# Optimization experiments

Measured on AMD Instinct MI355X. Metric: run time of the kernel, lower is better.

The kernel has to match this reference:

```python
import jax, jax.numpy as jnp
import numpy as np

B, L, D, H, OUT = 4, 2048, 1024, 8, 256
DH = D // H
EPS = 1e-12


def setup_inputs() -> dict:
    key = jax.random.key(0)
    ks = jax.random.split(key, 20)
    s = lambda fan_in: 1.0 / np.sqrt(fan_in)
    def lin(k, fin, fout):
        k1, k2 = jax.random.split(k)
        w = jax.random.uniform(k1, (fin, fout), jnp.float32, -s(fin), s(fin))
        b = jax.random.uniform(k2, (fout,), jnp.float32, -s(fin), s(fin))
        return w, b
    x = jax.random.normal(ks[0], (B, L, D), jnp.float32)
    wq, bq = lin(ks[1], D, D)
    wk, bk = lin(ks[2], D, D)
    wv, bv = lin(ks[3], D, D)
    gamma = jnp.ones((D,), jnp.float32)
    beta = jnp.zeros((D,), jnp.float32)
    wff, bff = lin(ks[4], D, D)
    wc1, bc1 = lin(ks[5], D, D)
    wc2, bc2 = lin(ks[6], D, 1)
    wl1, bl1 = lin(ks[7], L, L)
    wl2, bl2 = lin(ks[8], L, OUT)
    return dict(x=x, wq=wq, bq=bq, wk=wk, bk=bk, wv=wv, bv=bv,
                gamma=gamma, beta=beta, wff=wff, bff=bff,
                wc1=wc1, bc1=bc1, wc2=wc2, bc2=bc2,
                wl1=wl1, bl1=bl1, wl2=wl2, bl2=bl2)


def layernorm(x, gamma, beta):
    mean = x.mean(-1, keepdims=True)
    var = ((x - mean) ** 2).mean(-1, keepdims=True)  # biased variance
    return gamma * (x - mean) / jnp.sqrt(var + EPS) + beta


def reference(x, wq, bq, wk, bk, wv, bv, gamma, beta, wff, bff,
              wc1, bc1, wc2, bc2, wl1, bl1, wl2, bl2):
    # multi-head self-attention (dropout = identity at inference)
    q = (x @ wq + bq).reshape(B, L, H, DH)
    k = (x @ wk + bk).reshape(B, L, H, DH)
    v = (x @ wv + bv).reshape(B, L, H, DH)
    scores = jnp.einsum('bqhd,bkhd->bhqk', q, k) / np.sqrt(DH)
    attn = jax.nn.softmax(scores, axis=-1)                  # [B,H,L,L]
    ctx = jnp.einsum('bhqk,bkhd->bqhd', attn, v).reshape(B, L, D)
    h = layernorm(x + ctx, gamma, beta)
    # feedforward: Linear + ReLU (hidden = d_model), residual + same layernorm params
    ff = jax.nn.relu(h @ wff + bff)
    h = layernorm(h + ff, gamma, beta)
    # collapse d_model -> 1
    c = jax.nn.relu(h @ wc1 + bc1)
    c = jax.nn.relu(c @ wc2 + bc2)                          # [B,L,1]
    c = jnp.squeeze(c, axis=-1)                             # [B,L]
    # collapse length -> out_featuresize
    c = jax.nn.relu(c @ wl1 + bl1)
    out = c @ wl2 + bl2                                     # [B,OUT]
    return out
```

## Files before the change

### kernel.cpp

```cpp
#include <hip/hip_runtime.h>

typedef unsigned short u16;
typedef unsigned int u32;
typedef __attribute__((ext_vector_type(4))) float f32x4;
typedef __attribute__((ext_vector_type(8))) short short8;
typedef __attribute__((ext_vector_type(4))) u32 u32x4;
typedef __attribute__((ext_vector_type(4))) u16 u16x4;

#define BB 4
#define LL 2048
#define DD 1024
#define HH 8
#define DHH 128

__device__ __forceinline__ u16 f2b(float f) {
  u32 u = __builtin_bit_cast(u32, f);
  u += 0x7fffu + ((u >> 16) & 1u);
  return (u16)(u >> 16);
}
__device__ __forceinline__ float b2f(u16 h) {
  u32 u = ((u32)h) << 16;
  return __builtin_bit_cast(float, u);
}
__device__ __forceinline__ float exp2_fast(float x) {
  float r;
  asm("v_exp_f32 %0, %1" : "=v"(r) : "v"(x));
  return r;
}
__device__ __forceinline__ u32 packbf(float a, float b) {
  return (u32)f2b(a) | ((u32)f2b(b) << 16);
}
__device__ __forceinline__ u32 bperm(int srcLane, u32 v) {
  return (u32)__builtin_amdgcn_ds_bpermute(srcLane << 2, (int)v);
}

#define GLDS16(g, l)                                                          \
  __builtin_amdgcn_global_load_lds(                                           \
      (const __attribute__((address_space(1))) void*)(g),                     \
      (__attribute__((address_space(3))) void*)(l), 16, 0, 0)

__global__ __launch_bounds__(256) void cvt_k(const float* __restrict__ X,
                                             u16* __restrict__ Xb, long n) {
  long i = ((long)blockIdx.x * 256 + threadIdx.x) * 4;
  if (i >= n) return;
  f32x4 v = *(const f32x4*)(X + i);
  u16x4 o;
#pragma unroll
  for (int k = 0; k < 4; k++) o[k] = f2b(v[k]);
  *(u16x4*)(Xb + i) = o;
}

__global__ __launch_bounds__(256) void tr_k(const float* __restrict__ W,
                                            u16* __restrict__ WT) {
  __shared__ float tile[32][33];
  const int bx = blockIdx.x, by = blockIdx.y;
  const int tx = threadIdx.x & 31, ty = threadIdx.x >> 5;
#pragma unroll
  for (int i = 0; i < 4; i++)
    tile[ty + i * 8][tx] =
        W[(long)(by * 32 + ty + i * 8) * 1024 + bx * 32 + tx];
  __syncthreads();
#pragma unroll
  for (int i = 0; i < 4; i++)
    WT[(long)(bx * 32 + ty + i * 8) * 1024 + by * 32 + tx] =
        f2b(tile[tx][ty + i * 8]);
}

__global__ __launch_bounds__(256, 3) void qkv_k(
    const u16* __restrict__ A, const u16* __restrict__ QT,
    const u16* __restrict__ KT, const u16* __restrict__ VTw,
    const float* __restrict__ bq, const float* __restrict__ bk,
    const float* __restrict__ bv, float qscale, u16* __restrict__ Qo,
    u16* __restrict__ Ko, u16* __restrict__ Vo) {
  __shared__ u16 As[2][128 * 32];
  __shared__ u16 Bs[2][128 * 32];
  const int K = 1024;
  const int nwg = gridDim.x * gridDim.y;
  const int bid = blockIdx.x + blockIdx.y * gridDim.x;
  const int swz = (bid & 7) * (nwg >> 3) + (bid >> 3);
  const int bxi = swz % 24, byi = swz / 24;
  const int sector = bxi >> 3;
  const u16* BT = sector == 0 ? QT : (sector == 1 ? KT : VTw);
  const float* bias = sector == 0 ? bq : (sector == 1 ? bk : bv);
  const float scale = sector == 0 ? qscale : 1.f;
  const int t = threadIdx.x;
  const int l = t & 63, w = t >> 6;
  const int lr = l & 15, lg = l >> 4;
  const int wr = (w >> 1) * 64, wc = (w & 1) * 64;
  const long bm = (long)byi * 128, bn = (long)(bxi & 7) * 128;
  const int srow = l >> 2;
  const int scol = (l & 3) * 8;
  const u16* Ag0 = A + (bm + w * 32 + srow) * (long)K + scol;
  const u16* Ag1 = A + (bm + w * 32 + 16 + srow) * (long)K + scol;
  const u16* Bg0 = BT + (bn + w * 32 + srow) * (long)K + scol;
  const u16* Bg1 = BT + (bn + w * 32 + 16 + srow) * (long)K + scol;
  const int wo = w * 1024;
  f32x4 acc[4][4] = {};
  GLDS16(Ag0, &As[0][wo]);
  GLDS16(Ag1, &As[0][wo + 512]);
  GLDS16(Bg0, &Bs[0][wo]);
  GLDS16(Bg1, &Bs[0][wo + 512]);
  __syncthreads();
  int cur = 0;
  for (int k0 = 0; k0 < K; k0 += 32) {
    const int nxt = cur ^ 1;
    if (k0 + 32 < K) {
      GLDS16(Ag0 + k0 + 32, &As[nxt][wo]);
      GLDS16(Ag1 + k0 + 32, &As[nxt][wo + 512]);
      GLDS16(Bg0 + k0 + 32, &Bs[nxt][wo]);
      GLDS16(Bg1 + k0 + 32, &Bs[nxt][wo + 512]);
    }
    short8 af[4], bf[4];
#pragma unroll
    for (int i = 0; i < 4; i++)
      af[i] = *(const short8*)&As[cur][(wr + i * 16 + lr) * 32 + lg * 8];
#pragma unroll
    for (int i = 0; i < 4; i++)
      bf[i] = *(const short8*)&Bs[cur][(wc + i * 16 + lr) * 32 + lg * 8];
#pragma unroll
    for (int i = 0; i < 4; i++)
#pragma unroll
      for (int j = 0; j < 4; j++)
        acc[i][j] = __builtin_amdgcn_mfma_f32_16x16x32_bf16(af[i], bf[j],
                                                            acc[i][j], 0, 0, 0);
    __syncthreads();
    cur = nxt;
  }
#pragma unroll
  for (int i = 0; i < 4; i++)
#pragma unroll
    for (int j = 0; j < 4; j++) {
      long col = bn + wc + j * 16 + lr;
      float bvv = bias[col];
      if (sector == 2) {
        long row0 = bm + wr + i * 16 + lg * 4;
        long b = row0 >> 11, l0 = row0 & 2047;
        u16x4 ov;
#pragma unroll
        for (int r = 0; r < 4; r++) ov[r] = f2b(acc[i][j][r] + bvv);
        *(u16x4*)(Vo + (b * 1024 + col) * 2048 + l0) = ov;
      } else {
        u16* Out = sector == 0 ? Qo : Ko;
#pragma unroll
        for (int r = 0; r < 4; r++) {
          long row = bm + wr + i * 16 + lg * 4 + r;
          Out[row * 1024 + col] = f2b((acc[i][j][r] + bvv) * scale);
        }
      }
    }
}

template <bool RELU, int OMODE>
__global__ __launch_bounds__(256, 3) void gemm_k(
    const u16* __restrict__ A, const u16* __restrict__ BT,
    const float* __restrict__ bias, float scale, float* __restrict__ Cf,
    u16* __restrict__ Cb, const float* __restrict__ w2,
    float* __restrict__ cvec, int M, int N, int K) {
  __shared__ u16 As[2][128 * 32];
  __shared__ u16 Bs[2][128 * 32];
  const int nwg = gridDim.x * gridDim.y;
  const int bid = blockIdx.x + blockIdx.y * gridDim.x;
  const int swz = (bid & 7) * (nwg >> 3) + (bid >> 3);
  const int bxi = swz % gridDim.x, byi = swz / gridDim.x;
  const int t = threadIdx.x;
  const int l = t & 63, w = t >> 6;
  const int lr = l & 15, lg = l >> 4;
  const int wr = (w >> 1) * 64, wc = (w & 1) * 64;
  const long bm = (long)byi * 128, bn = (long)bxi * 128;
  const int srow = l >> 2;
  const int scol = (l & 3) * 8;
  const u16* Ag0 = A + (bm + w * 32 + srow) * (long)K + scol;
  const u16* Ag1 = A + (bm + w * 32 + 16 + srow) * (long)K + scol;
  const u16* Bg0 = BT + (bn + w * 32 + srow) * (long)K + scol;
  const u16* Bg1 = BT + (bn + w * 32 + 16 + srow) * (long)K + scol;
  const int wo = w * 1024;
  f32x4 acc[4][4] = {};
  GLDS16(Ag0, &As[0][wo]);
  GLDS16(Ag1, &As[0][wo + 512]);
  GLDS16(Bg0, &Bs[0][wo]);
  GLDS16(Bg1, &Bs[0][wo + 512]);
  __syncthreads();
  int cur = 0;
  for (int k0 = 0; k0 < K; k0 += 32) {
    const int nxt = cur ^ 1;
    if (k0 + 32 < K) {
      GLDS16(Ag0 + k0 + 32, &As[nxt][wo]);
      GLDS16(Ag1 + k0 + 32, &As[nxt][wo + 512]);
      GLDS16(Bg0 + k0 + 32, &Bs[nxt][wo]);
      GLDS16(Bg1 + k0 + 32, &Bs[nxt][wo + 512]);
    }
    short8 af[4], bf[4];
#pragma unroll
    for (int i = 0; i < 4; i++)
      af[i] = *(const short8*)&As[cur][(wr + i * 16 + lr) * 32 + lg * 8];
#pragma unroll
    for (int i = 0; i < 4; i++)
      bf[i] = *(const short8*)&Bs[cur][(wc + i * 16 + lr) * 32 + lg * 8];
#pragma unroll
    for (int i = 0; i < 4; i++)
#pragma unroll
      for (int j = 0; j < 4; j++)
        acc[i][j] = __builtin_amdgcn_mfma_f32_16x16x32_bf16(af[i], bf[j],
                                                            acc[i][j], 0, 0, 0);
    __syncthreads();
    cur = nxt;
  }
  if (OMODE == 3) {
    float bvj[4], w2j[4];
#pragma unroll
    for (int j = 0; j < 4; j++) {
      long col = bn + wc + j * 16 + lr;
      bvj[j] = bias[col];
      w2j[j] = w2[col];
    }
#pragma unroll
    for (int i = 0; i < 4; i++)
#pragma unroll
      for (int r = 0; r < 4; r++) {
        float a2 = 0.f;
#pragma unroll
        for (int j = 0; j < 4; j++)
          a2 += fmaxf(acc[i][j][r] + bvj[j], 0.f) * w2j[j];
        a2 += __shfl_xor(a2, 1, 64);
        a2 += __shfl_xor(a2, 2, 64);
        a2 += __shfl_xor(a2, 4, 64);
        a2 += __shfl_xor(a2, 8, 64);
        if (lr == 0) {
          long row = bm + wr + i * 16 + lg * 4 + r;
          atomicAdd(&cvec[row], a2);
        }
      }
  } else {
#pragma unroll
    for (int i = 0; i < 4; i++)
#pragma unroll
      for (int j = 0; j < 4; j++) {
        long col = bn + wc + j * 16 + lr;
        float bv = bias[col];
#pragma unroll
        for (int r = 0; r < 4; r++) {
          long row = bm + wr + i * 16 + lg * 4 + r;
          float v2 = (acc[i][j][r] + bv) * scale;
          if (RELU) v2 = fmaxf(v2, 0.f);
          Cf[row * N + col] = v2;
        }
      }
  }
}

__global__ __launch_bounds__(256, 2) void flash_k(const u16* __restrict__ Q,
                                                  const u16* __restrict__ Kb,
                                                  const u16* __restrict__ VT,
                                                  float* __restrict__ ctx) {
  __shared__ u16 Ks2[2][64 * 128];
  __shared__ u16 Vs2[2][128 * 64];
  const int nwg = gridDim.x * gridDim.y;
  const int bid = blockIdx.x + blockIdx.y * gridDim.x;
  const int swz = (bid & 7) * (nwg >> 3) + (bid >> 3);
  const int bxi = swz % gridDim.x, byi = swz / gridDim.x;
  const int t = threadIdx.x;
  const int l = t & 63, w = t >> 6;
  const int lr = l & 15, lg = l >> 4;
  const int b = byi >> 3, h = byi & 7;
  const long kbase = ((long)b * LL) * DD + h * DHH;
  const long vtbase = ((long)(b * 8 + h) * DHH) * LL;
  const int q0 = bxi * 128;

  short8 qf0[4], qf1[4];
  {
    const u16* qp0 = Q + kbase + (long)(q0 + w * 32 + lr) * DD + lg * 8;
    const u16* qp1 = qp0 + 16 * DD;
#pragma unroll
    for (int c = 0; c < 4; c++) {
      qf0[c] = *(const short8*)(qp0 + c * 32);
      qf1[c] = *(const short8*)(qp1 + c * 32);
    }
  }
  f32x4 oacc0[8] = {}, oacc1[8] = {};
  float mprev0 = -1e30f, mprev1 = -1e30f;
  float lsum0 = 0.f, lsum1 = 0.f;

  const u16* kg[4];
  const u16* vg[4];
  u16* kl[4];
  u16* vl[4];
#pragma unroll
  for (int i = 0; i < 4; i++) {
    int rk = w * 16 + 4 * i + (l >> 4);
    kg[i] = Kb + kbase + (long)rk * DD + ((l & 15) ^ (rk & 7)) * 8;
    kl[i] = &Ks2[0][(w * 16 + 4 * i) * 128];
    int rv = w * 32 + 8 * i + (l >> 3);
    vg[i] = VT + vtbase + (long)rv * LL + ((l & 7) ^ (rv & 7)) * 8;
    vl[i] = &Vs2[0][(w * 32 + 8 * i) * 64];
  }
#pragma unroll
  for (int i = 0; i < 4; i++) {
    GLDS16(kg[i], kl[i]);
    GLDS16(vg[i], vl[i]);
  }
  __syncthreads();

  int colk[4], colv[2];
#pragma unroll
  for (int c = 0; c < 4; c++) colk[c] = (((c * 4 + lg) ^ (lr & 7)) * 8);
#pragma unroll
  for (int kk = 0; kk < 2; kk++) colv[kk] = (((kk * 4 + lg) ^ (lr & 7)) * 8);

  const int NT = LL / 64;
  for (int it = 0; it < NT; ++it) {
    const int cur = it & 1;
    if (it + 1 < NT) {
      const int ko = (cur ^ 1) * (64 * 128);
      const int vo = (cur ^ 1) * (128 * 64);
#pragma unroll
      for (int i = 0; i < 4; i++) {
        kg[i] += 64 * DD;
        vg[i] += 64;
        GLDS16(kg[i], kl[i] + ko);
        GLDS16(vg[i], vl[i] + vo);
      }
    }
    const u16* Kc = &Ks2[cur][0];
    const u16* Vc = &Vs2[cur][0];

    f32x4 s0[4] = {}, s1[4] = {};
#pragma unroll
    for (int jc = 0; jc < 4; jc++)
#pragma unroll
      for (int c = 0; c < 4; c++) {
        short8 kf = *(const short8*)&Kc[(jc * 16 + lr) * 128 + colk[c]];
        s0[jc] =
            __builtin_amdgcn_mfma_f32_16x16x32_bf16(kf, qf0[c], s0[jc], 0, 0, 0);
        s1[jc] =
            __builtin_amdgcn_mfma_f32_16x16x32_bf16(kf, qf1[c], s1[jc], 0, 0, 0);
      }

    float mx0 = fmaxf(fmaxf(s0[0][0], s0[0][1]), fmaxf(s0[0][2], s0[0][3]));
    float mx1 = fmaxf(fmaxf(s1[0][0], s1[0][1]), fmaxf(s1[0][2], s1[0][3]));
#pragma unroll
    for (int jc = 1; jc < 4; jc++) {
      mx0 = fmaxf(mx0, fmaxf(fmaxf(s0[jc][0], s0[jc][1]),
                             fmaxf(s0[jc][2], s0[jc][3])));
      mx1 = fmaxf(mx1, fmaxf(fmaxf(s1[jc][0], s1[jc][1]),
                             fmaxf(s1[jc][2], s1[jc][3])));
    }
    mx0 = fmaxf(mx0, __shfl_xor(mx0, 16, 64));
    mx0 = fmaxf(mx0, __shfl_xor(mx0, 32, 64));
    mx1 = fmaxf(mx1, __shfl_xor(mx1, 16, 64));
    mx1 = fmaxf(mx1, __shfl_xor(mx1, 32, 64));

    if (__any((int)((mx0 > mprev0 + 8.f) || (mx1 > mprev1 + 8.f)))) {
      float mn0 = fmaxf(mprev0, mx0), mn1 = fmaxf(mprev1, mx1);
      float al0 = exp2_fast(mprev0 - mn0), al1 = exp2_fast(mprev1 - mn1);
      mprev0 = mn0;
      mprev1 = mn1;
      lsum0 *= al0;
      lsum1 *= al1;
      float ar0[4], ar1[4];
#pragma unroll
      for (int r = 0; r < 4; r++) {
        ar0[r] = __shfl(al0, lg * 4 + r, 64);
        ar1[r] = __shfl(al1, lg * 4 + r, 64);
      }
#pragma unroll
      for (int d8 = 0; d8 < 8; d8++)
#pragma unroll
        for (int r = 0; r < 4; r++) {
          oacc0[d8][r] *= ar0[r];
          oacc1[d8][r] *= ar1[r];
        }
    }

    u32 pk0[4][2], pk1[4][2];
    float la0 = 0.f, la1 = 0.f;
#pragma unroll
    for (int jc = 0; jc < 4; jc++) {
      float a0 = exp2_fast(s0[jc][0] - mprev0);
      float a1 = exp2_fast(s0[jc][1] - mprev0);
      float a2 = exp2_fast(s0[jc][2] - mprev0);
      float a3 = exp2_fast(s0[jc][3] - mprev0);
      la0 += (a0 + a1) + (a2 + a3);
      pk0[jc][0] = packbf(a0, a1);
      pk0[jc][1] = packbf(a2, a3);
      float b0 = exp2_fast(s1[jc][0] - mprev1);
      float b1 = exp2_fast(s1[jc][1] - mprev1);
      float b2 = exp2_fast(s1[jc][2] - mprev1);
      float b3 = exp2_fast(s1[jc][3] - mprev1);
      la1 += (b0 + b1) + (b2 + b3);
      pk1[jc][0] = packbf(b0, b1);
      pk1[jc][1] = packbf(b2, b3);
    }
    lsum0 += la0;
    lsum1 += la1;

    short8 pf0[2], pf1[2];
#pragma unroll
    for (int kk = 0; kk < 2; kk++) {
      u32x4 av0, av1;
#pragma unroll
      for (int m = 0; m < 4; m++) {
        int srcl = lr + ((((lg & 1) << 1) + (m >> 1)) << 4);
        u32 x0 = bperm(srcl, pk0[2 * kk][m & 1]);
        u32 x1 = bperm(srcl, pk0[2 * kk + 1][m & 1]);
        av0[m] = (lg >> 1) ? x1 : x0;
        u32 y0 = bperm(srcl, pk1[2 * kk][m & 1]);
        u32 y1 = bperm(srcl, pk1[2 * kk + 1][m & 1]);
        av1[m] = (lg >> 1) ? y1 : y0;
      }
      pf0[kk] = __builtin_bit_cast(short8, av0);
      pf1[kk] = __builtin_bit_cast(short8, av1);
    }

#pragma unroll
    for (int kk = 0; kk < 2; kk++)
#pragma unroll
      for (int d8 = 0; d8 < 8; d8++) {
        short8 vf = *(const short8*)&Vc[(d8 * 16 + lr) * 64 + colv[kk]];
        oacc0[d8] = __builtin_amdgcn_mfma_f32_16x16x32_bf16(pf0[kk], vf,
                                                            oacc0[d8], 0, 0, 0);
        oacc1[d8] = __builtin_amdgcn_mfma_f32_16x16x32_bf16(pf1[kk], vf,
                                                            oacc1[d8], 0, 0, 0);
      }
    __syncthreads();
  }

  lsum0 += __shfl_xor(lsum0, 16, 64);
  lsum0 += __shfl_xor(lsum0, 32, 64);
  lsum1 += __shfl_xor(lsum1, 16, 64);
  lsum1 += __shfl_xor(lsum1, 32, 64);
#pragma unroll
  for (int r = 0; r < 4; r++) {
    float inv0 = 1.f / __shfl(lsum0, lg * 4 + r, 64);
    float inv1 = 1.f / __shfl(lsum1, lg * 4 + r, 64);
    float* cp0 = ctx + kbase + (long)(q0 + w * 32 + lg * 4 + r) * DD;
    float* cp1 = cp0 + 16 * DD;
#pragma unroll
    for (int d8 = 0; d8 < 8; d8++) {
      cp0[d8 * 16 + lr] = oacc0[d8][r] * inv0;
      cp1[d8 * 16 + lr] = oacc1[d8][r] * inv1;
    }
  }
}

__global__ __launch_bounds__(256) void ln_k(const float* __restrict__ X,
                                            const float* __restrict__ R,
                                            const float* __restrict__ gamma,
                                            const float* __restrict__ beta,
                                            float* __restrict__ Hf,
                                            u16* __restrict__ Hb) {
  const int row = blockIdx.x, t = threadIdx.x;
  const long off = (long)row * DD + t * 4;
  f32x4 v = *(const f32x4*)(X + off);
  f32x4 rv = *(const f32x4*)(R + off);
#pragma unroll
  for (int i = 0; i < 4; i++) v[i] += rv[i];
  float s = v[0] + v[1] + v[2] + v[3];
  float q = v[0] * v[0] + v[1] * v[1] + v[2] * v[2] + v[3] * v[3];
#pragma unroll
  for (int m = 32; m >= 1; m >>= 1) {
    s += __shfl_xor(s, m, 64);
    q += __shfl_xor(q, m, 64);
  }
  __shared__ float red[8];
  if ((t & 63) == 0) {
    red[t >> 6] = s;
    red[4 + (t >> 6)] = q;
  }
  __syncthreads();
  s = red[0] + red[1] + red[2] + red[3];
  q = red[4] + red[5] + red[6] + red[7];
  const float mean = s * (1.f / 1024.f);
  const float var = q * (1.f / 1024.f) - mean * mean;
  const float rstd = rsqrtf(var + 1e-12f);
  f32x4 g = *(const f32x4*)(gamma + t * 4);
  f32x4 be = *(const f32x4*)(beta + t * 4);
  f32x4 o;
#pragma unroll
  for (int i = 0; i < 4; i++) o[i] = g[i] * (v[i] - mean) * rstd + be[i];
  if (Hf) *(f32x4*)(Hf + off) = o;
  if (Hb) {
    u16x4 ob;
#pragma unroll
    for (int i = 0; i < 4; i++) ob[i] = f2b(o[i]);
    *(u16x4*)(Hb + off) = ob;
  }
}

template <bool BR>
__global__ __launch_bounds__(256) void smm_part(const float* __restrict__ Cin,
                                                const float* __restrict__ W,
                                                float* __restrict__ P, int Lr,
                                                int N, int SL,
                                                const float* __restrict__ b0) {
  const int j = blockIdx.x * 256 + threadIdx.x;
  const int l0 = blockIdx.y * SL;
  const float bb = BR ? b0[0] : 0.f;
  float a0 = 0, a1 = 0, a2 = 0, a3 = 0;
  for (int ll = l0; ll < l0 + SL; ll++) {
    float wv = W[(long)ll * N + j];
    float c0 = Cin[ll], c1 = Cin[Lr + ll], c2 = Cin[2 * Lr + ll],
          c3 = Cin[3 * Lr + ll];
    if (BR) {
      c0 = fmaxf(c0 + bb, 0.f);
      c1 = fmaxf(c1 + bb, 0.f);
      c2 = fmaxf(c2 + bb, 0.f);
      c3 = fmaxf(c3 + bb, 0.f);
    }
    a0 += c0 * wv;
    a1 += c1 * wv;
    a2 += c2 * wv;
    a3 += c3 * wv;
  }
  float* Pp = P + ((long)blockIdx.y * 4) * N + j;
  Pp[0] = a0;
  Pp[N] = a1;
  Pp[2 * N] = a2;
  Pp[3 * N] = a3;
}

template <bool RELU>
__global__ __launch_bounds__(256) void smm_red(const float* __restrict__ P,
                                               const float* __restrict__ bias,
                                               float* __restrict__ Out, int N,
                                               int S) {
  const int j = blockIdx.x * 256 + threadIdx.x;
#pragma unroll
  for (int b = 0; b < 4; b++) {
    float a = 0;
    for (int s = 0; s < S; s++) a += P[((long)s * 4 + b) * N + j];
    a += bias[j];
    if (RELU) a = fmaxf(a, 0.f);
    Out[(long)b * N + j] = a;
  }
}

extern "C" void kernel_launch(void* const* d_in, const int* in_sizes, int n_in,
                              void* d_out, int out_size, void* d_ws,
                              size_t ws_size, hipStream_t stream) {
  (void)in_sizes; (void)n_in; (void)out_size; (void)ws_size;
  const float* x = (const float*)d_in[0];
  const float* wq = (const float*)d_in[1];
  const float* bq = (const float*)d_in[2];
  const float* wk = (const float*)d_in[3];
  const float* bk = (const float*)d_in[4];
  const float* wv = (const float*)d_in[5];
  const float* bv = (const float*)d_in[6];
  const float* gamma = (const float*)d_in[7];
  const float* beta = (const float*)d_in[8];
  const float* wff = (const float*)d_in[9];
  const float* bff = (const float*)d_in[10];
  const float* wc1 = (const float*)d_in[11];
  const float* bc1 = (const float*)d_in[12];
  const float* wc2 = (const float*)d_in[13];
  const float* bc2 = (const float*)d_in[14];
  const float* wl1 = (const float*)d_in[15];
  const float* bl1 = (const float*)d_in[16];
  const float* wl2 = (const float*)d_in[17];
  const float* bl2 = (const float*)d_in[18];

  char* wsp = (char*)d_ws;
  size_t off = 0;
  auto take = [&](size_t bytes) -> char* {
    char* p = wsp + off;
    off += (bytes + 255) & ~(size_t)255;
    return p;
  };
  u16* xb = (u16*)take((size_t)8192 * 1024 * 2);
  u16* wqT = (u16*)take((size_t)1024 * 1024 * 2);
  u16* wkT = (u16*)take((size_t)1024 * 1024 * 2);
  u16* wvT = (u16*)take((size_t)1024 * 1024 * 2);
  u16* wffT = (u16*)take((size_t)1024 * 1024 * 2);
  u16* wc1T = (u16*)take((size_t)1024 * 1024 * 2);
  u16* qb = (u16*)take((size_t)8192 * 1024 * 2);
  u16* kbuf = (u16*)take((size_t)8192 * 1024 * 2);
  u16* vT = (u16*)take((size_t)8192 * 1024 * 2);
  float* ctxb = (float*)take((size_t)8192 * 1024 * 4);
  float* h1f = (float*)take((size_t)8192 * 1024 * 4);
  float* cvec = (float*)take(8192 * 4);
  float* c3 = (float*)take(8192 * 4);
  float* P1 = (float*)take((size_t)16 * 4 * 2048 * 4);
  float* P2 = (float*)take((size_t)16 * 4 * 256 * 4);
  u16* h1b = qb;
  u16* h2b = kbuf;
  float* ff = ctxb;

  cvt_k<<<8192, 256, 0, stream>>>(x, xb, (long)8192 * 1024);
  dim3 trg(32, 32);
  tr_k<<<trg, 256, 0, stream>>>(wq, wqT);
  tr_k<<<trg, 256, 0, stream>>>(wk, wkT);
  tr_k<<<trg, 256, 0, stream>>>(wv, wvT);
  tr_k<<<trg, 256, 0, stream>>>(wff, wffT);
  tr_k<<<trg, 256, 0, stream>>>(wc1, wc1T);

  qkv_k<<<dim3(24, 64), 256, 0, stream>>>(xb, wqT, wkT, wvT, bq, bk, bv,
                                          0.12751743f, qb, kbuf, vT);
  flash_k<<<dim3(16, 32), 256, 0, stream>>>(qb, kbuf, vT, ctxb);
  ln_k<<<8192, 256, 0, stream>>>(x, ctxb, gamma, beta, h1f, h1b);
  dim3 gg(8, 64);
  gemm_k<true, 0><<<gg, 256, 0, stream>>>(h1b, wffT, bff, 1.f, ff, nullptr,
                                          nullptr, nullptr, 8192, 1024, 1024);
  ln_k<<<8192, 256, 0, stream>>>(h1f, ff, gamma, beta, nullptr, h2b);
  hipMemsetAsync(cvec, 0, 8192 * sizeof(float), stream);
  gemm_k<true, 3><<<gg, 256, 0, stream>>>(h2b, wc1T, bc1, 1.f, nullptr,
                                          nullptr, wc2, cvec, 8192, 1024,
                                          1024);
  smm_part<true><<<dim3(8, 16), 256, 0, stream>>>(cvec, wl1, P1, 2048, 2048,
                                                  128, bc2);
  smm_red<true><<<8, 256, 0, stream>>>(P1, bl1, c3, 2048, 16);
  smm_part<false><<<dim3(1, 16), 256, 0, stream>>>(c3, wl2, P2, 2048, 256,
                                                   128, nullptr);
  smm_red<false><<<1, 256, 0, stream>>>(P2, bl2, (float*)d_out, 256, 16);
}
```

Baseline: 378.0 us.

## Use 256x256-tile 8-wave GEMM mainloop with swizzled LDS and phased prefetch

```diff
diff --git a/kernel.cpp b/kernel.cpp
--- a/kernel.cpp
+++ b/kernel.cpp
@@ -39,6 +39,8 @@
       (const __attribute__((address_space(1))) void*)(g),                     \
       (__attribute__((address_space(3))) void*)(l), 16, 0, 0)
 
+#define MFMA_BF16 __builtin_amdgcn_mfma_f32_16x16x32_bf16
+
 __global__ __launch_bounds__(256) void cvt_k(const float* __restrict__ X,
                                              u16* __restrict__ Xb, long n) {
   long i = ((long)blockIdx.x * 256 + threadIdx.x) * 4;
@@ -66,74 +68,115 @@
         f2b(tile[tx][ty + i * 8]);
 }
 
-__global__ __launch_bounds__(256, 3) void qkv_k(
+__device__ __forceinline__ void g8_loop(const u16* __restrict__ A,
+                                        const u16* __restrict__ BT, long bm,
+                                        long bnr, u16* AsB, u16* BsB,
+                                        f32x4 (&acc)[8][4]) {
+  const int t = threadIdx.x;
+  const int l = t & 63, w = t >> 6;
+  const int lr = l & 15, lg = l >> 4;
+  const int wr2 = (w >> 2) * 128, wc2 = (w & 3) * 64;
+  const int rA = t >> 3;
+  const int swz = (t & 7) ^ (rA & 7);
+  const u16* gA = A + (bm + rA) * 1024 + swz * 8;
+  const u16* gB = BT + (bnr + rA) * 1024 + swz * 8;
+  u16* const dA = AsB + w * 512;
+  u16* const dB = BsB + w * 512;
+  int xk[2];
+  xk[0] = ((lg) ^ (lr & 7)) * 8;
+  xk[1] = ((4 + lg) ^ (lr & 7)) * 8;
+
+  auto STG = [&](int h, int nb, int kt) {
+    const u16* g = (h < 2) ? gA : gB;
+    u16* d = ((h < 2) ? dA : dB) + nb * 16384;
+    const int rb = (h & 1) * 128;
+    GLDS16(g + (long)rb * 1024 + kt * 64, d + rb * 64);
+    GLDS16(g + (long)(rb + 64) * 1024 + kt * 64, d + (rb + 64) * 64);
+  };
+
+#pragma unroll
+  for (int h = 0; h < 4; h++) STG(h, 0, 0);
+  asm volatile("s_waitcnt vmcnt(0)" ::: "memory");
+  __builtin_amdgcn_s_barrier();
+
+  short8 bf[4][2];
+  for (int kt = 0; kt < 16; ++kt) {
+    const int cur = kt & 1;
+    const u16* Ac = AsB + cur * 16384;
+    const u16* Bc = BsB + cur * 16384;
+#pragma unroll
+    for (int p = 0; p < 4; ++p) {
+      short8 af[2][2];
+#pragma unroll
+      for (int iq = 0; iq < 2; ++iq) {
+        const int arow = wr2 + (p * 2 + iq) * 16 + lr;
+#pragma unroll
+        for (int ks = 0; ks < 2; ks++)
+          af[iq][ks] = *(const short8*)&Ac[arow * 64 + xk[ks]];
+      }
+      if (p == 0) {
+#pragma unroll
+        for (int j = 0; j < 4; j++) {
+          const int brow = wc2 + j * 16 + lr;
+#pragma unroll
+          for (int ks = 0; ks < 2; ks++)
+            bf[j][ks] = *(const short8*)&Bc[brow * 64 + xk[ks]];
+        }
+      }
+      if (kt + 1 < 16) STG(p, cur ^ 1, kt + 1);
+      __builtin_amdgcn_s_barrier();
+      asm volatile("s_waitcnt lgkmcnt(0)" ::: "memory");
+      __builtin_amdgcn_sched_barrier(0);
+      __builtin_amdgcn_s_setprio(1);
+#pragma unroll
+      for (int iq = 0; iq < 2; ++iq) {
+        const int i = p * 2 + iq;
+#pragma unroll
+        for (int j = 0; j < 4; j++) {
+          acc[i][j] = MFMA_BF16(af[iq][0], bf[j][0], acc[i][j], 0, 0, 0);
+          acc[i][j] = MFMA_BF16(af[iq][1], bf[j][1], acc[i][j], 0, 0, 0);
+        }
+      }
+      __builtin_amdgcn_s_setprio(0);
+      if (p == 3) asm volatile("s_waitcnt vmcnt(0)" ::: "memory");
+      __builtin_amdgcn_s_barrier();
+    }
+  }
+}
+
+__global__ __launch_bounds__(512, 2) void qkv8_k(
     const u16* __restrict__ A, const u16* __restrict__ QT,
     const u16* __restrict__ KT, const u16* __restrict__ VTw,
     const float* __restrict__ bq, const float* __restrict__ bk,
     const float* __restrict__ bv, float qscale, u16* __restrict__ Qo,
     u16* __restrict__ Ko, u16* __restrict__ Vo) {
-  __shared__ u16 As[2][128 * 32];
-  __shared__ u16 Bs[2][128 * 32];
-  const int K = 1024;
+  __shared__ u16 As[2 * 16384];
+  __shared__ u16 Bs[2 * 16384];
   const int nwg = gridDim.x * gridDim.y;
   const int bid = blockIdx.x + blockIdx.y * gridDim.x;
-  const int swz = (bid & 7) * (nwg >> 3) + (bid >> 3);
-  const int bxi = swz % 24, byi = swz / 24;
-  const int sector = bxi >> 3;
+  const int swzb = (bid & 7) * (nwg >> 3) + (bid >> 3);
+  const int bxi = swzb % 12, byi = swzb / 12;
+  const int sector = bxi >> 2;
   const u16* BT = sector == 0 ? QT : (sector == 1 ? KT : VTw);
   const float* bias = sector == 0 ? bq : (sector == 1 ? bk : bv);
   const float scale = sector == 0 ? qscale : 1.f;
+  const long bm = (long)byi * 256;
+  const long bnl = (long)(bxi & 3) * 256;
+  f32x4 acc[8][4] = {};
+  g8_loop(A, BT, bm, bnl, As, Bs, acc);
+
   const int t = threadIdx.x;
   const int l = t & 63, w = t >> 6;
   const int lr = l & 15, lg = l >> 4;
-  const int wr = (w >> 1) * 64, wc = (w & 1) * 64;
-  const long bm = (long)byi * 128, bn = (long)(bxi & 7) * 128;
-  const int srow = l >> 2;
-  const int scol = (l & 3) * 8;
-  const u16* Ag0 = A + (bm + w * 32 + srow) * (long)K + scol;
-  const u16* Ag1 = A + (bm + w * 32 + 16 + srow) * (long)K + scol;
-  const u16* Bg0 = BT + (bn + w * 32 + srow) * (long)K + scol;
-  const u16* Bg1 = BT + (bn + w * 32 + 16 + srow) * (long)K + scol;
-  const int wo = w * 1024;
-  f32x4 acc[4][4] = {};
-  GLDS16(Ag0, &As[0][wo]);
-  GLDS16(Ag1, &As[0][wo + 512]);
-  GLDS16(Bg0, &Bs[0][wo]);
-  GLDS16(Bg1, &Bs[0][wo + 512]);
-  __syncthreads();
-  int cur = 0;
-  for (int k0 = 0; k0 < K; k0 += 32) {
-    const int nxt = cur ^ 1;
-    if (k0 + 32 < K) {
-      GLDS16(Ag0 + k0 + 32, &As[nxt][wo]);
-      GLDS16(Ag1 + k0 + 32, &As[nxt][wo + 512]);
-      GLDS16(Bg0 + k0 + 32, &Bs[nxt][wo]);
-      GLDS16(Bg1 + k0 + 32, &Bs[nxt][wo + 512]);
-    }
-    short8 af[4], bf[4];
-#pragma unroll
-    for (int i = 0; i < 4; i++)
-      af[i] = *(const short8*)&As[cur][(wr + i * 16 + lr) * 32 + lg * 8];
-#pragma unroll
-    for (int i = 0; i < 4; i++)
-      bf[i] = *(const short8*)&Bs[cur][(wc + i * 16 + lr) * 32 + lg * 8];
-#pragma unroll
-    for (int i = 0; i < 4; i++)
-#pragma unroll
-      for (int j = 0; j < 4; j++)
-        acc[i][j] = __builtin_amdgcn_mfma_f32_16x16x32_bf16(af[i], bf[j],
-                                                            acc[i][j], 0, 0, 0);
-    __syncthreads();
-    cur = nxt;
-  }
-#pragma unroll
-  for (int i = 0; i < 4; i++)
+  const int wr2 = (w >> 2) * 128, wc2 = (w & 3) * 64;
+#pragma unroll
+  for (int i = 0; i < 8; i++)
 #pragma unroll
     for (int j = 0; j < 4; j++) {
-      long col = bn + wc + j * 16 + lr;
+      long col = bnl + wc2 + j * 16 + lr;
       float bvv = bias[col];
       if (sector == 2) {
-        long row0 = bm + wr + i * 16 + lg * 4;
+        long row0 = bm + wr2 + i * 16 + lg * 4;
         long b = row0 >> 11, l0 = row0 & 2047;
         u16x4 ov;
 #pragma unroll
@@ -143,7 +186,7 @@
         u16* Out = sector == 0 ? Qo : Ko;
 #pragma unroll
         for (int r = 0; r < 4; r++) {
-          long row = bm + wr + i * 16 + lg * 4 + r;
+          long row = bm + wr2 + i * 16 + lg * 4 + r;
           Out[row * 1024 + col] = f2b((acc[i][j][r] + bvv) * scale);
         }
       }
@@ -151,70 +194,34 @@
 }
 
 template <bool RELU, int OMODE>
-__global__ __launch_bounds__(256, 3) void gemm_k(
+__global__ __launch_bounds__(512, 2) void gemm8_k(
     const u16* __restrict__ A, const u16* __restrict__ BT,
-    const float* __restrict__ bias, float scale, float* __restrict__ Cf,
-    u16* __restrict__ Cb, const float* __restrict__ w2,
-    float* __restrict__ cvec, int M, int N, int K) {
-  __shared__ u16 As[2][128 * 32];
-  __shared__ u16 Bs[2][128 * 32];
+    const float* __restrict__ bias, float* __restrict__ Cf,
+    const float* __restrict__ w2, float* __restrict__ cvec) {
+  __shared__ u16 As[2 * 16384];
+  __shared__ u16 Bs[2 * 16384];
   const int nwg = gridDim.x * gridDim.y;
   const int bid = blockIdx.x + blockIdx.y * gridDim.x;
-  const int swz = (bid & 7) * (nwg >> 3) + (bid >> 3);
-  const int bxi = swz % gridDim.x, byi = swz / gridDim.x;
+  const int swzb = (bid & 7) * (nwg >> 3) + (bid >> 3);
+  const int bxi = swzb % gridDim.x, byi = swzb / gridDim.x;
+  const long bm = (long)byi * 256, bn = (long)bxi * 256;
+  f32x4 acc[8][4] = {};
+  g8_loop(A, BT, bm, bn, As, Bs, acc);
+
   const int t = threadIdx.x;
   const int l = t & 63, w = t >> 6;
   const int lr = l & 15, lg = l >> 4;
-  const int wr = (w >> 1) * 64, wc = (w & 1) * 64;
-  const long bm = (long)byi * 128, bn = (long)bxi * 128;
-  const int srow = l >> 2;
-  const int scol = (l & 3) * 8;
-  const u16* Ag0 = A + (bm + w * 32 + srow) * (long)K + scol;
-  const u16* Ag1 = A + (bm + w * 32 + 16 + srow) * (long)K + scol;
-  const u16* Bg0 = BT + (bn + w * 32 + srow) * (long)K + scol;
-  const u16* Bg1 = BT + (bn + w * 32 + 16 + srow) * (long)K + scol;
-  const int wo = w * 1024;
-  f32x4 acc[4][4] = {};
-  GLDS16(Ag0, &As[0][wo]);
-  GLDS16(Ag1, &As[0][wo + 512]);
-  GLDS16(Bg0, &Bs[0][wo]);
-  GLDS16(Bg1, &Bs[0][wo + 512]);
-  __syncthreads();
-  int cur = 0;
-  for (int k0 = 0; k0 < K; k0 += 32) {
-    const int nxt = cur ^ 1;
-    if (k0 + 32 < K) {
-      GLDS16(Ag0 + k0 + 32, &As[nxt][wo]);
-      GLDS16(Ag1 + k0 + 32, &As[nxt][wo + 512]);
-      GLDS16(Bg0 + k0 + 32, &Bs[nxt][wo]);
-      GLDS16(Bg1 + k0 + 32, &Bs[nxt][wo + 512]);
-    }
-    short8 af[4], bf[4];
-#pragma unroll
-    for (int i = 0; i < 4; i++)
-      af[i] = *(const short8*)&As[cur][(wr + i * 16 + lr) * 32 + lg * 8];
-#pragma unroll
-    for (int i = 0; i < 4; i++)
-      bf[i] = *(const short8*)&Bs[cur][(wc + i * 16 + lr) * 32 + lg * 8];
-#pragma unroll
-    for (int i = 0; i < 4; i++)
-#pragma unroll
-      for (int j = 0; j < 4; j++)
-        acc[i][j] = __builtin_amdgcn_mfma_f32_16x16x32_bf16(af[i], bf[j],
-                                                            acc[i][j], 0, 0, 0);
-    __syncthreads();
-    cur = nxt;
-  }
+  const int wr2 = (w >> 2) * 128, wc2 = (w & 3) * 64;
   if (OMODE == 3) {
     float bvj[4], w2j[4];
 #pragma unroll
     for (int j = 0; j < 4; j++) {
-      long col = bn + wc + j * 16 + lr;
+      long col = bn + wc2 + j * 16 + lr;
       bvj[j] = bias[col];
       w2j[j] = w2[col];
     }
 #pragma unroll
-    for (int i = 0; i < 4; i++)
+    for (int i = 0; i < 8; i++)
 #pragma unroll
       for (int r = 0; r < 4; r++) {
         float a2 = 0.f;
@@ -226,23 +233,23 @@
         a2 += __shfl_xor(a2, 4, 64);
         a2 += __shfl_xor(a2, 8, 64);
         if (lr == 0) {
-          long row = bm + wr + i * 16 + lg * 4 + r;
+          long row = bm + wr2 + i * 16 + lg * 4 + r;
           atomicAdd(&cvec[row], a2);
         }
       }
   } else {
 #pragma unroll
-    for (int i = 0; i < 4; i++)
+    for (int i = 0; i < 8; i++)
 #pragma unroll
       for (int j = 0; j < 4; j++) {
-        long col = bn + wc + j * 16 + lr;
+        long col = bn + wc2 + j * 16 + lr;
         float bv = bias[col];
 #pragma unroll
         for (int r = 0; r < 4; r++) {
-          long row = bm + wr + i * 16 + lg * 4 + r;
-          float v2 = (acc[i][j][r] + bv) * scale;
+          long row = bm + wr2 + i * 16 + lg * 4 + r;
+          float v2 = acc[i][j][r] + bv;
           if (RELU) v2 = fmaxf(v2, 0.f);
-          Cf[row * N + col] = v2;
+          Cf[row * 1024 + col] = v2;
         }
       }
   }
@@ -329,10 +336,8 @@
 #pragma unroll
       for (int c = 0; c < 4; c++) {
         short8 kf = *(const short8*)&Kc[(jc * 16 + lr) * 128 + colk[c]];
-        s0[jc] =
-            __builtin_amdgcn_mfma_f32_16x16x32_bf16(kf, qf0[c], s0[jc], 0, 0, 0);
-        s1[jc] =
-            __builtin_amdgcn_mfma_f32_16x16x32_bf16(kf, qf1[c], s1[jc], 0, 0, 0);
+        s0[jc] = MFMA_BF16(kf, qf0[c], s0[jc], 0, 0, 0);
+        s1[jc] = MFMA_BF16(kf, qf1[c], s1[jc], 0, 0, 0);
       }
 
     float mx0 = fmaxf(fmaxf(s0[0][0], s0[0][1]), fmaxf(s0[0][2], s0[0][3]));
@@ -416,10 +421,8 @@
 #pragma unroll
       for (int d8 = 0; d8 < 8; d8++) {
         short8 vf = *(const short8*)&Vc[(d8 * 16 + lr) * 64 + colv[kk]];
-        oacc0[d8] = __builtin_amdgcn_mfma_f32_16x16x32_bf16(pf0[kk], vf,
-                                                            oacc0[d8], 0, 0, 0);
-        oacc1[d8] = __builtin_amdgcn_mfma_f32_16x16x32_bf16(pf1[kk], vf,
-                                                            oacc1[d8], 0, 0, 0);
+        oacc0[d8] = MFMA_BF16(pf0[kk], vf, oacc0[d8], 0, 0, 0);
+        oacc1[d8] = MFMA_BF16(pf1[kk], vf, oacc1[d8], 0, 0, 0);
       }
     __syncthreads();
   }
@@ -592,18 +595,16 @@
   tr_k<<<trg, 256, 0, stream>>>(wff, wffT);
   tr_k<<<trg, 256, 0, stream>>>(wc1, wc1T);
 
-  qkv_k<<<dim3(24, 64), 256, 0, stream>>>(xb, wqT, wkT, wvT, bq, bk, bv,
-                                          0.12751743f, qb, kbuf, vT);
+  qkv8_k<<<dim3(12, 32), 512, 0, stream>>>(xb, wqT, wkT, wvT, bq, bk, bv,
+                                           0.12751743f, qb, kbuf, vT);
   flash_k<<<dim3(16, 32), 256, 0, stream>>>(qb, kbuf, vT, ctxb);
   ln_k<<<8192, 256, 0, stream>>>(x, ctxb, gamma, beta, h1f, h1b);
-  dim3 gg(8, 64);
-  gemm_k<true, 0><<<gg, 256, 0, stream>>>(h1b, wffT, bff, 1.f, ff, nullptr,
-                                          nullptr, nullptr, 8192, 1024, 1024);
+  gemm8_k<true, 0><<<dim3(4, 32), 512, 0, stream>>>(h1b, wffT, bff, ff,
+                                                    nullptr, nullptr);
   ln_k<<<8192, 256, 0, stream>>>(h1f, ff, gamma, beta, nullptr, h2b);
   hipMemsetAsync(cvec, 0, 8192 * sizeof(float), stream);
-  gemm_k<true, 3><<<gg, 256, 0, stream>>>(h2b, wc1T, bc1, 1.f, nullptr,
-                                          nullptr, wc2, cvec, 8192, 1024,
-                                          1024);
+  gemm8_k<true, 3><<<dim3(4, 32), 512, 0, stream>>>(h2b, wc1T, bc1, nullptr,
+                                                    wc2, cvec);
   smm_part<true><<<dim3(8, 16), 256, 0, stream>>>(cvec, wl1, P1, 2048, 2048,
                                                   128, bc2);
   smm_red<true><<<8, 256, 0, stream>>>(P1, bl1, c3, 2048, 16);
```

Result: slower. 411.3 us (+8.8%).
